# Performance work log

Hardware: AMD Instinct MI355X
Metric: run time of the kernel (lower is better)

## Reference

```python
import jax, jax.numpy as jnp
import numpy as np

IMG = 256                      # image_size
FOV_RAD = float(np.radians(90.0))
CAM_RANGE = 3.0
AGENT_RADIUS = 0.05
OBSTACLE_HEIGHT = 0.5          # obstacle_base_height
AGENT_HEIGHT = 0.2             # hard-coded in render_depth_from_position
MAX_R = IMG // 4               # max pixel_radius clamp
P = 2 * MAX_R + 1              # rasterization patch side


def setup_inputs() -> dict:
    key = jax.random.key(0)
    k1, k2, k3, k4 = jax.random.split(key, 4)
    agent_pos = jax.random.normal(k1, (2,), dtype=jnp.float32) * 0.5
    goal_pos = jax.random.normal(k2, (2,), dtype=jnp.float32) * 0.5 + jnp.array([0.0, 1.5], jnp.float32)
    other_agents = jax.random.uniform(k3, (2047, 2), dtype=jnp.float32, minval=-2.0, maxval=2.0)
    u = jax.random.uniform(k4, (2048, 3), dtype=jnp.float32)
    # obstacle positions in [-2,2]^2, radii in [0.05, 0.30]
    obstacles = jnp.concatenate([u[:, :2] * 4.0 - 2.0, 0.05 + 0.25 * u[:, 2:3]], axis=1)
    return {"agent_pos": agent_pos, "goal_pos": goal_pos,
            "other_agents": other_agents, "obstacles": obstacles}


def _forward(agent_pos, goal_pos, other_agents, obstacles):
    # --- camera rotation from view direction (goal - agent) ---
    view = goal_pos - agent_pos
    view = view / (jnp.linalg.norm(view) + 1e-8)
    c, s = view[1], view[0]
    rot = jnp.stack([jnp.stack([c, s]), jnp.stack([-s, c])])  # [2,2]

    n_ag = other_agents.shape[0]
    n_ob = obstacles.shape[0]
    positions = jnp.concatenate([other_agents, obstacles[:, :2]], axis=0)          # [N,2]
    radii = jnp.concatenate([jnp.full((n_ag,), AGENT_RADIUS, jnp.float32),
                             obstacles[:, 2]])                                     # [N]
    heights = jnp.concatenate([jnp.full((n_ag,), AGENT_HEIGHT, jnp.float32),
                               jnp.full((n_ob,), OBSTACLE_HEIGHT, jnp.float32)])   # [N]

    # --- project all objects at once ---
    rel = positions - agent_pos                 # [N,2]
    cam = rel @ rot.T                           # cam[:,0]=x (lateral), cam[:,1]=y (forward)
    cam_x, cam_y = cam[:, 0], cam[:, 1]
    dist = jnp.sqrt(cam_x * cam_x + cam_y * cam_y)
    angle = jnp.arctan2(cam_x, cam_y)
    valid = (cam_y >= 0.0) & (dist <= CAM_RANGE) & (jnp.abs(angle) <= FOV_RAD / 2)

    pixel_x = angle / (FOV_RAD / 2) * 0.5
    px_int = jnp.floor((pixel_x + 0.5) * IMG).astype(jnp.int32)          # int() trunc; arg >= 0 when valid
    pr = jnp.floor(radii / (dist + 1e-8) * IMG * 0.5).astype(jnp.int32)  # pixel radius
    pr = jnp.clip(pr, 1, MAX_R)

    depth = jnp.minimum(dist / CAM_RANGE, 1.0) * (1.0 - heights * 0.3)
    depth = jnp.maximum(depth, 0.0)
    depth = jnp.where(valid, depth, 1.0)        # invalid objects are no-ops under min

    # --- rasterize disks via parallel scatter-min ---
    d = jnp.arange(-MAX_R, MAX_R + 1, dtype=jnp.int32)
    dy = d[:, None]                             # [P,1]
    dx = d[None, :]                             # [1,P]
    disk = (dx * dx + dy * dy)[None, :, :] <= (pr * pr)[:, None, None]   # [N,P,P]
    py = IMG // 2 + dy                          # [P,1]
    px = px_int[:, None, None] + dx             # [N,P,P]
    inb = (py >= 0) & (py < IMG) & (px >= 0) & (px < IMG)
    mask = disk & inb & valid[:, None, None]
    vals = jnp.where(mask, depth[:, None, None], 1.0)                    # [N,P,P]
    flat = jnp.clip(py, 0, IMG - 1) * IMG + jnp.clip(px, 0, IMG - 1)     # [N,P,P]

    img = jnp.ones((IMG * IMG,), jnp.float32)
    img = img.at[flat.reshape(-1)].min(vals.reshape(-1))
    return img.reshape(1, IMG, IMG)


def reference(agent_pos, goal_pos, other_agents, obstacles):
    return _forward(agent_pos, goal_pos, other_agents, obstacles)
```

## Files before the change

### kernel.cpp

```cpp
#include <hip/hip_runtime.h>
#include <math.h>

#define IMG 256
#define MAX_R 64

__global__ void init_img_kernel(float4* __restrict__ img4) {
    int i = blockIdx.x * blockDim.x + threadIdx.x;
    if (i < (IMG * IMG) / 4) {
        img4[i] = make_float4(1.0f, 1.0f, 1.0f, 1.0f);
    }
}

__global__ __launch_bounds__(256) void render_kernel(
    const float* __restrict__ agent_pos,
    const float* __restrict__ goal_pos,
    const float* __restrict__ other_agents,
    const float* __restrict__ obstacles,
    unsigned int* __restrict__ img,
    int n_ag, int n_ob)
{
    const int e = blockIdx.x;
    if (e >= n_ag + n_ob) return;

    const float ax = agent_pos[0], ay = agent_pos[1];
    const float gx = goal_pos[0], gy = goal_pos[1];
    const float vx = gx - ax, vy = gy - ay;
    const float nrm = sqrtf(vx * vx + vy * vy) + 1e-8f;
    const float s = vx / nrm;
    const float c = vy / nrm;

    float ex, ey, radius, height;
    if (e < n_ag) {
        ex = other_agents[2 * e];
        ey = other_agents[2 * e + 1];
        radius = 0.05f;
        height = 0.2f;
    } else {
        const int o = e - n_ag;
        ex = obstacles[3 * o];
        ey = obstacles[3 * o + 1];
        radius = obstacles[3 * o + 2];
        height = 0.5f;
    }

    const float rx = ex - ax, ry = ey - ay;
    const float cx = rx * c + ry * s;
    const float cy = ry * c - rx * s;
    const float dist = sqrtf(cx * cx + cy * cy);
    const float angle = (float)atan2((double)cx, (double)cy);

    const float half_fov = 0.78539816339744830962f;
    const bool valid = (cy >= 0.0f) && (dist <= 3.0f) && (fabsf(angle) <= half_fov);
    if (!valid) return;

    const float pixel_x = angle / half_fov * 0.5f;
    const int px_int = (int)floorf((pixel_x + 0.5f) * 256.0f);

    int pr = (int)floorf(radius / (dist + 1e-8f) * 256.0f * 0.5f);
    pr = min(max(pr, 1), MAX_R);

    float depth = fminf(dist / 3.0f, 1.0f) * (1.0f - height * 0.3f);
    depth = fmaxf(depth, 0.0f);
    const unsigned int dbits = __float_as_uint(depth);

    const int side = 2 * pr + 1;
    const int total = side * side;
    const int rr = pr * pr;
    for (int i = threadIdx.x; i < total; i += blockDim.x) {
        const int row = i / side;
        const int col = i - row * side;
        const int dy = row - pr;
        const int dx = col - pr;
        if (dx * dx + dy * dy <= rr) {
            const int py = 128 + dy;
            const int px = px_int + dx;
            if (px >= 0 && px < IMG && py >= 0 && py < IMG) {
                atomicMin(&img[py * IMG + px], dbits);
            }
        }
    }
}

extern "C" void kernel_launch(void* const* d_in, const int* in_sizes, int n_in,
                              void* d_out, int out_size, void* d_ws, size_t ws_size,
                              hipStream_t stream) {
    const float* agent_pos    = (const float*)d_in[0];
    const float* goal_pos     = (const float*)d_in[1];
    const float* other_agents = (const float*)d_in[2];
    const float* obstacles    = (const float*)d_in[3];

    const int n_ag = in_sizes[2] / 2;
    const int n_ob = in_sizes[3] / 3;

    float* img = (float*)d_out;

    init_img_kernel<<<(IMG * IMG / 4 + 255) / 256, 256, 0, stream>>>((float4*)img);
    render_kernel<<<n_ag + n_ob, 256, 0, stream>>>(
        agent_pos, goal_pos, other_agents, obstacles,
        (unsigned int*)img, n_ag, n_ob);
}
```

Measured before the change: 74.78 us.

## Replace per-object atomic scatter with compaction plus per-pixel gather rasterization

A single-block kernel projects all objects, culls invalid ones, and compacts the visible disk parameters (center x, radius squared, depth) into a workspace list through a shared-memory counter. A second kernel then assigns one thread per pixel, loops over the compacted list and keeps the minimum depth of the disks that cover it, writing each pixel exactly once. This removes the image init pass, the per-object blocks and the global atomicMin traffic. In exchange every pixel in the central band scans the whole visible list serially, and the compaction runs on only one block.

```diff
diff --git a/kernel.cpp b/kernel.cpp
--- a/kernel.cpp
+++ b/kernel.cpp
@@ -4,23 +4,19 @@
 #define IMG 256
 #define MAX_R 64
 
-__global__ void init_img_kernel(float4* __restrict__ img4) {
-    int i = blockIdx.x * blockDim.x + threadIdx.x;
-    if (i < (IMG * IMG) / 4) {
-        img4[i] = make_float4(1.0f, 1.0f, 1.0f, 1.0f);
-    }
-}
 
-__global__ __launch_bounds__(256) void render_kernel(
+__global__ __launch_bounds__(1024) void compact_kernel(
     const float* __restrict__ agent_pos,
     const float* __restrict__ goal_pos,
     const float* __restrict__ other_agents,
     const float* __restrict__ obstacles,
-    unsigned int* __restrict__ img,
+    unsigned int* __restrict__ count_out,
+    int4* __restrict__ params,
     int n_ag, int n_ob)
 {
-    const int e = blockIdx.x;
-    if (e >= n_ag + n_ob) return;
+    __shared__ unsigned int cnt;
+    if (threadIdx.x == 0) cnt = 0;
+    __syncthreads();
 
     const float ax = agent_pos[0], ay = agent_pos[1];
     const float gx = goal_pos[0], gy = goal_pos[1];
@@ -29,56 +25,72 @@
     const float s = vx / nrm;
     const float c = vy / nrm;
 
-    float ex, ey, radius, height;
-    if (e < n_ag) {
-        ex = other_agents[2 * e];
-        ey = other_agents[2 * e + 1];
-        radius = 0.05f;
-        height = 0.2f;
-    } else {
-        const int o = e - n_ag;
-        ex = obstacles[3 * o];
-        ey = obstacles[3 * o + 1];
-        radius = obstacles[3 * o + 2];
-        height = 0.5f;
+    const int n_total = n_ag + n_ob;
+    for (int e = threadIdx.x; e < n_total; e += blockDim.x) {
+        float ex, ey, radius, height;
+        if (e < n_ag) {
+            ex = other_agents[2 * e];
+            ey = other_agents[2 * e + 1];
+            radius = 0.05f;
+            height = 0.2f;
+        } else {
+            const int o = e - n_ag;
+            ex = obstacles[3 * o];
+            ey = obstacles[3 * o + 1];
+            radius = obstacles[3 * o + 2];
+            height = 0.5f;
+        }
+
+        const float rx = ex - ax, ry = ey - ay;
+        const float cx = rx * c + ry * s;
+        const float cy = ry * c - rx * s;
+        const float dist = sqrtf(cx * cx + cy * cy);
+        const float angle = (float)atan2((double)cx, (double)cy);
+
+        const float half_fov = 0.78539816339744830962f;
+        const bool valid = (cy >= 0.0f) && (dist <= 3.0f) && (fabsf(angle) <= half_fov);
+        if (!valid) continue;
+
+        const float pixel_x = angle / half_fov * 0.5f;
+        const int px_int = (int)floorf((pixel_x + 0.5f) * 256.0f);
+
+        int pr = (int)floorf(radius / (dist + 1e-8f) * 256.0f * 0.5f);
+        pr = min(max(pr, 1), MAX_R);
+
+        float depth = fminf(dist / 3.0f, 1.0f) * (1.0f - height * 0.3f);
+        depth = fmaxf(depth, 0.0f);
+
+        const unsigned int idx = atomicAdd(&cnt, 1u);
+        params[idx] = make_int4(px_int, pr * pr, __float_as_int(depth), 0);
     }
 
-    const float rx = ex - ax, ry = ey - ay;
-    const float cx = rx * c + ry * s;
-    const float cy = ry * c - rx * s;
-    const float dist = sqrtf(cx * cx + cy * cy);
-    const float angle = (float)atan2((double)cx, (double)cy);
+    __syncthreads();
+    if (threadIdx.x == 0) *count_out = cnt;
+}
 
-    const float half_fov = 0.78539816339744830962f;
-    const bool valid = (cy >= 0.0f) && (dist <= 3.0f) && (fabsf(angle) <= half_fov);
-    if (!valid) return;
+__global__ __launch_bounds__(256) void raster_kernel(
+    const unsigned int* __restrict__ count_in,
+    const int4* __restrict__ params,
+    float* __restrict__ img)
+{
+    const int row = blockIdx.x;
+    const int px  = threadIdx.x;
+    const int dy  = row - 128;
+    const int dy2 = dy * dy;
 
-    const float pixel_x = angle / half_fov * 0.5f;
-    const int px_int = (int)floorf((pixel_x + 0.5f) * 256.0f);
-
-    int pr = (int)floorf(radius / (dist + 1e-8f) * 256.0f * 0.5f);
-    pr = min(max(pr, 1), MAX_R);
-
-    float depth = fminf(dist / 3.0f, 1.0f) * (1.0f - height * 0.3f);
-    depth = fmaxf(depth, 0.0f);
-    const unsigned int dbits = __float_as_uint(depth);
-
-    const int side = 2 * pr + 1;
-    const int total = side * side;
-    const int rr = pr * pr;
-    for (int i = threadIdx.x; i < total; i += blockDim.x) {
-        const int row = i / side;
-        const int col = i - row * side;
-        const int dy = row - pr;
-        const int dx = col - pr;
-        if (dx * dx + dy * dy <= rr) {
-            const int py = 128 + dy;
-            const int px = px_int + dx;
-            if (px >= 0 && px < IMG && py >= 0 && py < IMG) {
-                atomicMin(&img[py * IMG + px], dbits);
+    float dmin = 1.0f;
+    if (dy >= -MAX_R && dy <= MAX_R) {
+        const int n = (int)(*count_in);
+        for (int i = 0; i < n; ++i) {
+            const int4 p = params[i];
+            if (dy2 <= p.y) {
+                const int dx = px - p.x;
+                const int m  = dx * dx + dy2;
+                if (m <= p.y) dmin = fminf(dmin, __int_as_float(p.z));
             }
         }
     }
+    img[row * IMG + px] = dmin;
 }
 
 extern "C" void kernel_launch(void* const* d_in, const int* in_sizes, int n_in,
@@ -92,10 +104,12 @@
     const int n_ag = in_sizes[2] / 2;
     const int n_ob = in_sizes[3] / 3;
 
-    float* img = (float*)d_out;
+    unsigned int* count = (unsigned int*)d_ws;
+    int4* params = (int4*)((char*)d_ws + 16);
 
-    init_img_kernel<<<(IMG * IMG / 4 + 255) / 256, 256, 0, stream>>>((float4*)img);
-    render_kernel<<<n_ag + n_ob, 256, 0, stream>>>(
+    compact_kernel<<<1, 1024, 0, stream>>>(
         agent_pos, goal_pos, other_agents, obstacles,
-        (unsigned int*)img, n_ag, n_ob);
+        count, params, n_ag, n_ob);
+
+    raster_kernel<<<IMG, 256, 0, stream>>>(count, params, (float*)d_out);
 }
```

New measurement: 142.9 us. 91.1% more time.
